# Kernel tuning notes

Hardware: AMD Instinct MI355X
Metric: run time of the kernel (lower is better)

## Reference

```python
import jax, jax.numpy as jnp
import numpy as np

B, IN, OUT = 8192, 4096, 4096
EPS = 1e-4


def setup_inputs() -> dict:
    key = jax.random.key(0)
    k1, k2 = jax.random.split(key)
    x = jax.random.normal(k1, (B, IN), dtype=jnp.float32)
    gamma = jnp.ones((IN,), dtype=jnp.float32)
    beta = jnp.zeros((IN,), dtype=jnp.float32)
    weight = jax.random.normal(k2, (OUT, IN), dtype=jnp.float32) * 0.02
    bias = jnp.zeros((OUT,), dtype=jnp.float32)
    return {"x": x, "gamma": gamma, "beta": beta, "weight": weight, "bias": bias}


def bin_weight(w):
    # center per output row, clamp, L1-scale, sign (2D branch of BinWeightFn)
    wc = jnp.clip(w - jnp.mean(w, axis=1, keepdims=True), -1.0, 1.0)
    n = w.shape[1]
    scale = jnp.sum(jnp.abs(wc), axis=1, keepdims=True) / n  # [out, 1]
    return jnp.sign(wc), scale


def reference(x, gamma, beta, weight, bias):
    # BatchNorm1d in training mode: batch statistics (biased variance)
    mu = jnp.mean(x, axis=0)
    var = jnp.var(x, axis=0)
    xn = (x - mu) / jnp.sqrt(var + EPS) * gamma + beta
    # binarize activations and weights
    x_bin = jnp.sign(xn)
    w_bin, scale = bin_weight(weight)
    # binary GEMM + bias, then per-output-channel L1 scale, then ReLU
    y = x_bin @ w_bin.T + bias          # [B, OUT]
    y = y * scale.reshape(1, -1)
    return jax.nn.relu(y)
```

## Files before the change

### kernel.cpp

```cpp
#include <hip/hip_runtime.h>
#include <stdint.h>

#define BATCH 8192
#define IN 4096
#define OUT 4096
#define EPS 1e-4f
#define RCHUNK 128
#define NCHUNKS (BATCH / RCHUNK)

typedef int v4i __attribute__((ext_vector_type(4)));
typedef unsigned char u8;

#define AS1(p) ((const __attribute__((address_space(1))) void*)(p))
#define AS3(p) ((__attribute__((address_space(3))) void*)(p))

__global__ __launch_bounds__(256) void colstat_partial(
    const float* __restrict__ x, float* __restrict__ P1, float* __restrict__ P2) {
    int c4 = blockIdx.x * 256 + threadIdx.x;
    int r0 = blockIdx.y * RCHUNK;
    float4 s1 = {0.f, 0.f, 0.f, 0.f}, s2 = {0.f, 0.f, 0.f, 0.f};
    const float4* p = (const float4*)x + (size_t)r0 * (IN / 4) + c4;
    for (int r = 0; r < RCHUNK; ++r) {
        float4 v = p[(size_t)r * (IN / 4)];
        s1.x += v.x; s1.y += v.y; s1.z += v.z; s1.w += v.w;
        s2.x += v.x * v.x; s2.y += v.y * v.y; s2.z += v.z * v.z; s2.w += v.w * v.w;
    }
    ((float4*)P1)[blockIdx.y * (IN / 4) + c4] = s1;
    ((float4*)P2)[blockIdx.y * (IN / 4) + c4] = s2;
}

__global__ __launch_bounds__(256) void colstat_final(
    const float* __restrict__ P1, const float* __restrict__ P2,
    const float* __restrict__ gamma, float* __restrict__ mu, float* __restrict__ aArr) {
    int col = blockIdx.x * 256 + threadIdx.x;
    double s1 = 0.0, s2 = 0.0;
    for (int c = 0; c < NCHUNKS; ++c) {
        s1 += (double)P1[c * IN + col];
        s2 += (double)P2[c * IN + col];
    }
    double m = s1 / (double)BATCH;
    double var = s2 / (double)BATCH - m * m;
    float rstd = (float)(1.0 / sqrt(var + (double)EPS));
    mu[col] = (float)m;
    aArr[col] = rstd * gamma[col];
}

__global__ __launch_bounds__(256) void binx8(
    const float* __restrict__ x, const float* __restrict__ mu,
    const float* __restrict__ aArr, const float* __restrict__ beta,
    u8* __restrict__ x01, int* __restrict__ px) {
    __shared__ int red[4];
    int r = blockIdx.x;
    int tid = threadIdx.x;
    int lane = tid & 63;
    int wv = tid >> 6;
    const float4* row = (const float4*)(x + (size_t)r * IN);
    const float4* m4 = (const float4*)mu;
    const float4* a4 = (const float4*)aArr;
    const float4* b4 = (const float4*)beta;
    uchar4* o4 = (uchar4*)(x01 + (size_t)r * IN);
    int cnt = 0;
#pragma unroll
    for (int it = 0; it < IN / 1024; ++it) {
        int q = it * 256 + tid;
        float4 v = row[q];
        float4 m = m4[q];
        float4 a = a4[q];
        float4 b = b4[q];
        uchar4 ob;
        ob.x = (u8)((v.x - m.x) * a.x + b.x > 0.f);
        ob.y = (u8)((v.y - m.y) * a.y + b.y > 0.f);
        ob.z = (u8)((v.z - m.z) * a.z + b.z > 0.f);
        ob.w = (u8)((v.w - m.w) * a.w + b.w > 0.f);
        cnt += (int)ob.x + (int)ob.y + (int)ob.z + (int)ob.w;
        o4[q] = ob;
    }
    for (int off = 32; off > 0; off >>= 1) cnt += __shfl_down(cnt, off, 64);
    if (lane == 0) red[wv] = cnt;
    __syncthreads();
    if (tid == 0) px[r] = red[0] + red[1] + red[2] + red[3];
}

__global__ __launch_bounds__(256) void binw8(
    const float* __restrict__ w, u8* __restrict__ w01,
    float* __restrict__ scale, int* __restrict__ pw) {
    __shared__ double redd[4];
    __shared__ int redi[4];
    __shared__ double bcast;
    int o = blockIdx.x;
    int tid = threadIdx.x;
    int lane = tid & 63;
    int wv = tid >> 6;
    const float4* row = (const float4*)(w + (size_t)o * IN);
    uchar4* o4 = (uchar4*)(w01 + (size_t)o * IN);

    float4 vs[4];
    float part = 0.f;
#pragma unroll
    for (int it = 0; it < 4; ++it) {
        vs[it] = row[it * 256 + tid];
        part += vs[it].x + vs[it].y + vs[it].z + vs[it].w;
    }
    double d = (double)part;
    for (int off = 32; off > 0; off >>= 1) d += __shfl_down(d, off, 64);
    if (lane == 0) redd[wv] = d;
    __syncthreads();
    if (tid == 0) bcast = (redd[0] + redd[1] + redd[2] + redd[3]) / (double)IN;
    __syncthreads();
    float mean = (float)bcast;

    float absacc = 0.f;
    int cnt = 0;
#pragma unroll
    for (int it = 0; it < 4; ++it) {
        float4 v = vs[it];
        float wcx = v.x - mean, wcy = v.y - mean, wcz = v.z - mean, wcw = v.w - mean;
        uchar4 ob;
        ob.x = (u8)(wcx > 0.f);
        ob.y = (u8)(wcy > 0.f);
        ob.z = (u8)(wcz > 0.f);
        ob.w = (u8)(wcw > 0.f);
        cnt += (int)ob.x + (int)ob.y + (int)ob.z + (int)ob.w;
        absacc += fminf(fabsf(wcx), 1.0f) + fminf(fabsf(wcy), 1.0f) +
                  fminf(fabsf(wcz), 1.0f) + fminf(fabsf(wcw), 1.0f);
        o4[it * 256 + tid] = ob;
    }
    double da = (double)absacc;
    for (int off = 32; off > 0; off >>= 1) da += __shfl_down(da, off, 64);
    for (int off = 32; off > 0; off >>= 1) cnt += __shfl_down(cnt, off, 64);
    if (lane == 0) { redd[wv] = da; redi[wv] = cnt; }
    __syncthreads();
    if (tid == 0) {
        scale[o] = (float)((redd[0] + redd[1] + redd[2] + redd[3]) / (double)IN);
        pw[o] = redi[0] + redi[1] + redi[2] + redi[3];
    }
}

#define BKB 128
#define NKT (IN / BKB)
#define NIT (NKT / 2)

#define STG_A(t, q, p) __builtin_amdgcn_global_load_lds( \
    AS1(ag + (size_t)((q)*64 + slr) * IN + (t)*BKB + sswz), \
    AS3(lds + (p)*65536 + (q)*8192 + sdst), 16, 0, 0)
#define STG_B(t, q, p) __builtin_amdgcn_global_load_lds( \
    AS1(bg + (size_t)((q)*64 + slr) * IN + (t)*BKB + sswz), \
    AS3(lds + (p)*65536 + 32768 + (q)*8192 + sdst), 16, 0, 0)

#define LOADA(p, rh) do { \
    _Pragma("unroll") for (int i_ = 0; i_ < 4; ++i_) \
    _Pragma("unroll") for (int k_ = 0; k_ < 2; ++k_) \
        af[i_][k_] = *(const v4i*)(lds + (p)*65536 + aBase + (rh)*8192 + i_*2048 + swk[k_]); \
} while (0)
#define LOADB(p, ch) do { \
    _Pragma("unroll") for (int j_ = 0; j_ < 2; ++j_) \
    _Pragma("unroll") for (int k_ = 0; k_ < 2; ++k_) \
        bf[j_][k_] = *(const v4i*)(lds + (p)*65536 + bBase + (ch)*4096 + j_*2048 + swk[k_]); \
} while (0)
#define MMA(rh, ch) do { \
    __builtin_amdgcn_s_setprio(1); \
    _Pragma("unroll") for (int i_ = 0; i_ < 4; ++i_) \
    _Pragma("unroll") for (int j_ = 0; j_ < 2; ++j_) \
    _Pragma("unroll") for (int k_ = 0; k_ < 2; ++k_) \
        acc[(rh)*4 + i_][(ch)*2 + j_] = __builtin_amdgcn_mfma_i32_16x16x64_i8( \
            af[i_][k_], bf[j_][k_], acc[(rh)*4 + i_][(ch)*2 + j_], 0, 0, 0); \
    __builtin_amdgcn_s_setprio(0); \
} while (0)
#define BAR() asm volatile("s_barrier" ::: "memory")
#define VM(n) asm volatile("s_waitcnt vmcnt(" #n ")" ::: "memory")

__global__ __launch_bounds__(512, 2) void bgemm_i8(
    const u8* __restrict__ x01, const u8* __restrict__ w01,
    const int* __restrict__ px, const int* __restrict__ pw,
    const float* __restrict__ scale, const float* __restrict__ bias,
    float* __restrict__ out) {
    __shared__ u8 lds[131072];

    int tid = threadIdx.x;
    int lane = tid & 63;
    int wave = tid >> 6;
    int wm = wave >> 2;
    int wn = wave & 3;

    int lin = blockIdx.y * (OUT / 256) + blockIdx.x;
    int swz = (lin & 7) * 64 + (lin >> 3);
    int colBlk = (swz & 15) * 256;
    int rowBlk = (swz >> 4) * 256;

    const u8* ag = x01 + (size_t)rowBlk * IN;
    const u8* bg = w01 + (size_t)colBlk * IN;

    int slr = tid >> 3;
    int ss = tid & 7;
    int sswz = (ss ^ (slr & 7)) * 16;
    int sdst = slr * 128 + ss * 16;

    int lrow = lane & 15;
    int lhi = lane >> 4;
    int llo = lane & 7;
    int swk[2] = { ((lhi) ^ llo) * 16, ((4 + lhi) ^ llo) * 16 };
    int aBase = (wm * 128 + lrow) * 128;
    int bBase = 32768 + (wn * 64 + lrow) * 128;

    v4i acc[8][4];
#pragma unroll
    for (int i = 0; i < 8; ++i)
#pragma unroll
        for (int j = 0; j < 4; ++j) acc[i][j] = (v4i){0, 0, 0, 0};
    v4i af[4][2], bf[2][2];

    STG_A(0, 0, 0); STG_A(0, 1, 0); STG_A(0, 2, 0); STG_A(0, 3, 0);
    STG_B(0, 0, 0); STG_B(0, 1, 0); STG_B(0, 2, 0); STG_B(0, 3, 0);
    STG_A(1, 0, 1); STG_A(1, 2, 1);
    VM(2);
    BAR();

    for (int j = 0; j < NIT - 1; ++j) {
        int O = 2 * j + 1, E2 = 2 * j + 2, O2 = 2 * j + 3;
        LOADA(0, 0); LOADB(0, 0);
        STG_B(O, 0, 1); STG_B(O, 1, 1);
        BAR(); MMA(0, 0); BAR();
        LOADB(0, 1);
        STG_B(O, 2, 1); STG_B(O, 3, 1);
        BAR(); MMA(0, 1); VM(6); BAR();
        LOADA(0, 1); LOADB(0, 0);
        STG_A(O, 1, 1); STG_A(O, 3, 1); STG_A(E2, 0, 0); STG_A(E2, 2, 0);
        BAR(); MMA(1, 0); BAR();
        LOADB(0, 1);
        BAR(); MMA(1, 1); VM(4); BAR();
        LOADA(1, 0); LOADB(1, 0);
        STG_B(E2, 0, 0); STG_B(E2, 1, 0);
        BAR(); MMA(0, 0); BAR();
        LOADB(1, 1);
        STG_B(E2, 2, 0); STG_B(E2, 3, 0);
        BAR(); MMA(0, 1); VM(4); BAR();
        LOADA(1, 1); LOADB(1, 0);
        STG_A(E2, 1, 0); STG_A(E2, 3, 0);
        BAR(); MMA(1, 0); BAR();
        LOADB(1, 1);
        STG_A(O2, 0, 1); STG_A(O2, 2, 1);
        BAR(); MMA(1, 1); VM(4); BAR();
    }

    {
        int O = NKT - 1;
        LOADA(0, 0); LOADB(0, 0);
        STG_B(O, 0, 1); STG_B(O, 1, 1);
        BAR(); MMA(0, 0); BAR();
        LOADB(0, 1);
        STG_B(O, 2, 1); STG_B(O, 3, 1);
        BAR(); MMA(0, 1); VM(6); BAR();
        LOADA(0, 1); LOADB(0, 0);
        STG_A(O, 1, 1); STG_A(O, 3, 1);
        BAR(); MMA(1, 0); BAR();
        LOADB(0, 1);
        BAR(); MMA(1, 1); VM(2); BAR();
        LOADA(1, 0); LOADB(1, 0);
        BAR(); MMA(0, 0); BAR();
        LOADB(1, 1);
        BAR(); MMA(0, 1); VM(0); BAR();
        LOADA(1, 1); LOADB(1, 0);
        BAR(); MMA(1, 0); BAR();
        LOADB(1, 1);
        BAR(); MMA(1, 1); BAR();
    }

    int crow0 = lhi * 4;
    int ccol = lrow;
#pragma unroll
    for (int i = 0; i < 8; ++i) {
        int rbase = rowBlk + wm * 128 + i * 16 + crow0;
        int pxr[4];
#pragma unroll
        for (int rg = 0; rg < 4; ++rg) pxr[rg] = px[rbase + rg];
#pragma unroll
        for (int j = 0; j < 4; ++j) {
            int cb = colBlk + wn * 64 + j * 16 + ccol;
            float sc = scale[cb];
            float bs = bias[cb];
            int pwc = pw[cb];
#pragma unroll
            for (int rg = 0; rg < 4; ++rg) {
                int dot = 4 * acc[i][j][rg] - 2 * pxr[rg] - 2 * pwc + IN;
                float y = ((float)dot + bs) * sc;
                out[(size_t)(rbase + rg) * OUT + cb] = y > 0.f ? y : 0.f;
            }
        }
    }
}

extern "C" void kernel_launch(void* const* d_in, const int* in_sizes, int n_in,
                              void* d_out, int out_size, void* d_ws, size_t ws_size,
                              hipStream_t stream) {
    const float* x = (const float*)d_in[0];
    const float* gamma = (const float*)d_in[1];
    const float* beta = (const float*)d_in[2];
    const float* weight = (const float*)d_in[3];
    const float* bias = (const float*)d_in[4];
    float* out = (float*)d_out;

    char* w = (char*)d_ws;
    float* mu = (float*)(w);
    float* aArr = (float*)(w + 16384);
    float* scale = (float*)(w + 32768);
    int* px = (int*)(w + 49152);
    int* pw = (int*)(w + 81920);
    float* P1 = (float*)(w + (1 << 20));
    float* P2 = (float*)(w + (2 << 20));
    u8* x01 = (u8*)(w + (4 << 20));
    u8* w01 = (u8*)(w + (36 << 20));

    colstat_partial<<<dim3(IN / 1024, NCHUNKS), 256, 0, stream>>>(x, P1, P2);
    colstat_final<<<dim3(IN / 256), 256, 0, stream>>>(P1, P2, gamma, mu, aArr);
    binx8<<<dim3(BATCH), 256, 0, stream>>>(x, mu, aArr, beta, x01, px);
    binw8<<<dim3(OUT), 256, 0, stream>>>(weight, w01, scale, pw);
    bgemm_i8<<<dim3(OUT / 256, BATCH / 256), 512, 0, stream>>>(x01, w01, px, pw, scale, bias, out);
}
```

Measured before the change: 412.2 us.

## Merge binarize kernels, reorder GEMM staging, use nontemporal output stores

```diff
diff --git a/kernel.cpp b/kernel.cpp
--- a/kernel.cpp
+++ b/kernel.cpp
@@ -20,6 +20,7 @@
     int r0 = blockIdx.y * RCHUNK;
     float4 s1 = {0.f, 0.f, 0.f, 0.f}, s2 = {0.f, 0.f, 0.f, 0.f};
     const float4* p = (const float4*)x + (size_t)r0 * (IN / 4) + c4;
+#pragma unroll 8
     for (int r = 0; r < RCHUNK; ++r) {
         float4 v = p[(size_t)r * (IN / 4)];
         s1.x += v.x; s1.y += v.y; s1.z += v.z; s1.w += v.w;
@@ -34,6 +35,7 @@
     const float* __restrict__ gamma, float* __restrict__ mu, float* __restrict__ aArr) {
     int col = blockIdx.x * 256 + threadIdx.x;
     double s1 = 0.0, s2 = 0.0;
+#pragma unroll 4
     for (int c = 0; c < NCHUNKS; ++c) {
         s1 += (double)P1[c * IN + col];
         s2 += (double)P2[c * IN + col];
@@ -45,94 +47,91 @@
     aArr[col] = rstd * gamma[col];
 }
 
-__global__ __launch_bounds__(256) void binx8(
+__global__ __launch_bounds__(256) void binxw(
     const float* __restrict__ x, const float* __restrict__ mu,
     const float* __restrict__ aArr, const float* __restrict__ beta,
-    u8* __restrict__ x01, int* __restrict__ px) {
-    __shared__ int red[4];
-    int r = blockIdx.x;
+    const float* __restrict__ w,
+    u8* __restrict__ x01, int* __restrict__ px,
+    u8* __restrict__ w01, float* __restrict__ scale, int* __restrict__ pw) {
+    __shared__ double redd[4];
+    __shared__ int redi[4];
+    __shared__ double bcast;
     int tid = threadIdx.x;
     int lane = tid & 63;
     int wv = tid >> 6;
-    const float4* row = (const float4*)(x + (size_t)r * IN);
-    const float4* m4 = (const float4*)mu;
-    const float4* a4 = (const float4*)aArr;
-    const float4* b4 = (const float4*)beta;
-    uchar4* o4 = (uchar4*)(x01 + (size_t)r * IN);
-    int cnt = 0;
-#pragma unroll
-    for (int it = 0; it < IN / 1024; ++it) {
-        int q = it * 256 + tid;
-        float4 v = row[q];
-        float4 m = m4[q];
-        float4 a = a4[q];
-        float4 b = b4[q];
-        uchar4 ob;
-        ob.x = (u8)((v.x - m.x) * a.x + b.x > 0.f);
-        ob.y = (u8)((v.y - m.y) * a.y + b.y > 0.f);
-        ob.z = (u8)((v.z - m.z) * a.z + b.z > 0.f);
-        ob.w = (u8)((v.w - m.w) * a.w + b.w > 0.f);
-        cnt += (int)ob.x + (int)ob.y + (int)ob.z + (int)ob.w;
-        o4[q] = ob;
-    }
-    for (int off = 32; off > 0; off >>= 1) cnt += __shfl_down(cnt, off, 64);
-    if (lane == 0) red[wv] = cnt;
-    __syncthreads();
-    if (tid == 0) px[r] = red[0] + red[1] + red[2] + red[3];
-}
-
-__global__ __launch_bounds__(256) void binw8(
-    const float* __restrict__ w, u8* __restrict__ w01,
-    float* __restrict__ scale, int* __restrict__ pw) {
-    __shared__ double redd[4];
-    __shared__ int redi[4];
-    __shared__ double bcast;
-    int o = blockIdx.x;
-    int tid = threadIdx.x;
-    int lane = tid & 63;
-    int wv = tid >> 6;
-    const float4* row = (const float4*)(w + (size_t)o * IN);
-    uchar4* o4 = (uchar4*)(w01 + (size_t)o * IN);
-
-    float4 vs[4];
-    float part = 0.f;
-#pragma unroll
-    for (int it = 0; it < 4; ++it) {
-        vs[it] = row[it * 256 + tid];
-        part += vs[it].x + vs[it].y + vs[it].z + vs[it].w;
-    }
-    double d = (double)part;
-    for (int off = 32; off > 0; off >>= 1) d += __shfl_down(d, off, 64);
-    if (lane == 0) redd[wv] = d;
-    __syncthreads();
-    if (tid == 0) bcast = (redd[0] + redd[1] + redd[2] + redd[3]) / (double)IN;
-    __syncthreads();
-    float mean = (float)bcast;
-
-    float absacc = 0.f;
-    int cnt = 0;
-#pragma unroll
-    for (int it = 0; it < 4; ++it) {
-        float4 v = vs[it];
-        float wcx = v.x - mean, wcy = v.y - mean, wcz = v.z - mean, wcw = v.w - mean;
-        uchar4 ob;
-        ob.x = (u8)(wcx > 0.f);
-        ob.y = (u8)(wcy > 0.f);
-        ob.z = (u8)(wcz > 0.f);
-        ob.w = (u8)(wcw > 0.f);
-        cnt += (int)ob.x + (int)ob.y + (int)ob.z + (int)ob.w;
-        absacc += fminf(fabsf(wcx), 1.0f) + fminf(fabsf(wcy), 1.0f) +
-                  fminf(fabsf(wcz), 1.0f) + fminf(fabsf(wcw), 1.0f);
-        o4[it * 256 + tid] = ob;
-    }
-    double da = (double)absacc;
-    for (int off = 32; off > 0; off >>= 1) da += __shfl_down(da, off, 64);
-    for (int off = 32; off > 0; off >>= 1) cnt += __shfl_down(cnt, off, 64);
-    if (lane == 0) { redd[wv] = da; redi[wv] = cnt; }
-    __syncthreads();
-    if (tid == 0) {
-        scale[o] = (float)((redd[0] + redd[1] + redd[2] + redd[3]) / (double)IN);
-        pw[o] = redi[0] + redi[1] + redi[2] + redi[3];
+
+    if (blockIdx.x < OUT) {
+        int o = blockIdx.x;
+        const float4* row = (const float4*)(w + (size_t)o * IN);
+        uchar4* o4 = (uchar4*)(w01 + (size_t)o * IN);
+
+        float4 vs[4];
+        float part = 0.f;
+#pragma unroll
+        for (int it = 0; it < 4; ++it) {
+            vs[it] = row[it * 256 + tid];
+            part += vs[it].x + vs[it].y + vs[it].z + vs[it].w;
+        }
+        double d = (double)part;
+        for (int off = 32; off > 0; off >>= 1) d += __shfl_down(d, off, 64);
+        if (lane == 0) redd[wv] = d;
+        __syncthreads();
+        if (tid == 0) bcast = (redd[0] + redd[1] + redd[2] + redd[3]) / (double)IN;
+        __syncthreads();
+        float mean = (float)bcast;
+
+        float absacc = 0.f;
+        int cnt = 0;
+#pragma unroll
+        for (int it = 0; it < 4; ++it) {
+            float4 v = vs[it];
+            float wcx = v.x - mean, wcy = v.y - mean, wcz = v.z - mean, wcw = v.w - mean;
+            uchar4 ob;
+            ob.x = (u8)(wcx > 0.f);
+            ob.y = (u8)(wcy > 0.f);
+            ob.z = (u8)(wcz > 0.f);
+            ob.w = (u8)(wcw > 0.f);
+            cnt += (int)ob.x + (int)ob.y + (int)ob.z + (int)ob.w;
+            absacc += fminf(fabsf(wcx), 1.0f) + fminf(fabsf(wcy), 1.0f) +
+                      fminf(fabsf(wcz), 1.0f) + fminf(fabsf(wcw), 1.0f);
+            o4[it * 256 + tid] = ob;
+        }
+        double da = (double)absacc;
+        for (int off = 32; off > 0; off >>= 1) da += __shfl_down(da, off, 64);
+        for (int off = 32; off > 0; off >>= 1) cnt += __shfl_down(cnt, off, 64);
+        if (lane == 0) { redd[wv] = da; redi[wv] = cnt; }
+        __syncthreads();
+        if (tid == 0) {
+            scale[o] = (float)((redd[0] + redd[1] + redd[2] + redd[3]) / (double)IN);
+            pw[o] = redi[0] + redi[1] + redi[2] + redi[3];
+        }
+    } else {
+        int r = blockIdx.x - OUT;
+        const float4* row = (const float4*)(x + (size_t)r * IN);
+        const float4* m4 = (const float4*)mu;
+        const float4* a4 = (const float4*)aArr;
+        const float4* b4 = (const float4*)beta;
+        uchar4* o4 = (uchar4*)(x01 + (size_t)r * IN);
+        int cnt = 0;
+#pragma unroll
+        for (int it = 0; it < IN / 1024; ++it) {
+            int q = it * 256 + tid;
+            float4 v = row[q];
+            float4 m = m4[q];
+            float4 a = a4[q];
+            float4 b = b4[q];
+            uchar4 ob;
+            ob.x = (u8)((v.x - m.x) * a.x + b.x > 0.f);
+            ob.y = (u8)((v.y - m.y) * a.y + b.y > 0.f);
+            ob.z = (u8)((v.z - m.z) * a.z + b.z > 0.f);
+            ob.w = (u8)((v.w - m.w) * a.w + b.w > 0.f);
+            cnt += (int)ob.x + (int)ob.y + (int)ob.z + (int)ob.w;
+            o4[q] = ob;
+        }
+        for (int off = 32; off > 0; off >>= 1) cnt += __shfl_down(cnt, off, 64);
+        if (lane == 0) redi[wv] = cnt;
+        __syncthreads();
+        if (tid == 0) px[r] = redi[0] + redi[1] + redi[2] + redi[3];
     }
 }
 
@@ -209,49 +208,52 @@
         for (int j = 0; j < 4; ++j) acc[i][j] = (v4i){0, 0, 0, 0};
     v4i af[4][2], bf[2][2];
 
-    STG_A(0, 0, 0); STG_A(0, 1, 0); STG_A(0, 2, 0); STG_A(0, 3, 0);
-    STG_B(0, 0, 0); STG_B(0, 1, 0); STG_B(0, 2, 0); STG_B(0, 3, 0);
+    STG_A(0, 0, 0); STG_A(0, 2, 0);
+    STG_A(0, 1, 0); STG_A(0, 3, 0);
+    STG_B(0, 0, 0); STG_B(0, 1, 0);
+    STG_B(0, 2, 0); STG_B(0, 3, 0);
     STG_A(1, 0, 1); STG_A(1, 2, 1);
     VM(2);
     BAR();
 
     for (int j = 0; j < NIT - 1; ++j) {
         int O = 2 * j + 1, E2 = 2 * j + 2, O2 = 2 * j + 3;
+        STG_B(O, 0, 1); STG_B(O, 1, 1);
         LOADA(0, 0); LOADB(0, 0);
-        STG_B(O, 0, 1); STG_B(O, 1, 1);
         BAR(); MMA(0, 0); BAR();
+        STG_B(O, 2, 1); STG_B(O, 3, 1);
         LOADB(0, 1);
-        STG_B(O, 2, 1); STG_B(O, 3, 1);
-        BAR(); MMA(0, 1); VM(6); BAR();
+        BAR(); MMA(0, 1); VM(10); BAR();
+        STG_A(O, 1, 1); STG_A(O, 3, 1);
         LOADA(0, 1); LOADB(0, 0);
-        STG_A(O, 1, 1); STG_A(O, 3, 1); STG_A(E2, 0, 0); STG_A(E2, 2, 0);
         BAR(); MMA(1, 0); BAR();
+        STG_A(E2, 0, 0); STG_A(E2, 2, 0);
         LOADB(0, 1);
         BAR(); MMA(1, 1); VM(4); BAR();
+        STG_A(E2, 1, 0); STG_A(E2, 3, 0);
         LOADA(1, 0); LOADB(1, 0);
+        BAR(); MMA(0, 0); BAR();
         STG_B(E2, 0, 0); STG_B(E2, 1, 0);
-        BAR(); MMA(0, 0); BAR();
         LOADB(1, 1);
+        BAR(); MMA(0, 1); VM(6); BAR();
         STG_B(E2, 2, 0); STG_B(E2, 3, 0);
-        BAR(); MMA(0, 1); VM(4); BAR();
         LOADA(1, 1); LOADB(1, 0);
-        STG_A(E2, 1, 0); STG_A(E2, 3, 0);
         BAR(); MMA(1, 0); BAR();
+        STG_A(O2, 0, 1); STG_A(O2, 2, 1);
         LOADB(1, 1);
-        STG_A(O2, 0, 1); STG_A(O2, 2, 1);
-        BAR(); MMA(1, 1); VM(4); BAR();
+        BAR(); MMA(1, 1); VM(2); BAR();
     }
 
     {
         int O = NKT - 1;
+        STG_B(O, 0, 1); STG_B(O, 1, 1);
         LOADA(0, 0); LOADB(0, 0);
-        STG_B(O, 0, 1); STG_B(O, 1, 1);
         BAR(); MMA(0, 0); BAR();
+        STG_B(O, 2, 1); STG_B(O, 3, 1);
         LOADB(0, 1);
-        STG_B(O, 2, 1); STG_B(O, 3, 1);
-        BAR(); MMA(0, 1); VM(6); BAR();
+        BAR(); MMA(0, 1); VM(10); BAR();
+        STG_A(O, 1, 1); STG_A(O, 3, 1);
         LOADA(0, 1); LOADB(0, 0);
-        STG_A(O, 1, 1); STG_A(O, 3, 1);
         BAR(); MMA(1, 0); BAR();
         LOADB(0, 1);
         BAR(); MMA(1, 1); VM(2); BAR();
@@ -283,7 +285,8 @@
             for (int rg = 0; rg < 4; ++rg) {
                 int dot = 4 * acc[i][j][rg] - 2 * pxr[rg] - 2 * pwc + IN;
                 float y = ((float)dot + bs) * sc;
-                out[(size_t)(rbase + rg) * OUT + cb] = y > 0.f ? y : 0.f;
+                __builtin_nontemporal_store(y > 0.f ? y : 0.f,
+                                            &out[(size_t)(rbase + rg) * OUT + cb]);
             }
         }
     }
@@ -312,7 +315,7 @@
 
     colstat_partial<<<dim3(IN / 1024, NCHUNKS), 256, 0, stream>>>(x, P1, P2);
     colstat_final<<<dim3(IN / 256), 256, 0, stream>>>(P1, P2, gamma, mu, aArr);
-    binx8<<<dim3(BATCH), 256, 0, stream>>>(x, mu, aArr, beta, x01, px);
-    binw8<<<dim3(OUT), 256, 0, stream>>>(weight, w01, scale, pw);
+    binxw<<<dim3(OUT + BATCH), 256, 0, stream>>>(x, mu, aArr, beta, weight,
+                                                 x01, px, w01, scale, pw);
     bgemm_i8<<<dim3(OUT / 256, BATCH / 256), 512, 0, stream>>>(x01, w01, px, pw, scale, bias, out);
 }
```

After: 417.7 us. About the same (+1.3%).
